# Kernel tuning notes

Hardware: AMD Instinct MI355X
Metric: run time of the kernel (lower is better)

## Reference

```python
import jax, jax.numpy as jnp
import numpy as np

N = 100000   # nodes
E = 1600000  # edges
B = 256      # graphs
EPS = 1e-5   # batchnorm eps


def setup_inputs() -> dict:
    key = jax.random.key(0)
    ks = jax.random.split(key, 20)
    inp = {
        "x": jax.random.normal(ks[0], (N, 22), dtype=jnp.float32),
        "edge_index": jax.random.randint(ks[1], (2, E), 0, N, dtype=jnp.int64),
        "batch": jnp.sort(jax.random.randint(ks[2], (N,), 0, B, dtype=jnp.int64)),
        # GCNConv weights (x @ W + b convention)
        "W1": jax.random.normal(ks[3], (22, 64), dtype=jnp.float32) * 0.2,
        "b1": jnp.zeros((64,), dtype=jnp.float32),
        "W2": jax.random.normal(ks[4], (64, 64), dtype=jnp.float32) * 0.12,
        "b2": jnp.zeros((64,), dtype=jnp.float32),
        "W3": jax.random.normal(ks[5], (64, 128), dtype=jnp.float32) * 0.12,
        "b3": jnp.zeros((128,), dtype=jnp.float32),
        # BatchNorm1d params + running stats (eval mode)
        "g1": jax.random.uniform(ks[6], (64,), minval=0.5, maxval=1.5),
        "be1": jax.random.normal(ks[7], (64,)) * 0.1,
        "m1": jax.random.normal(ks[8], (64,)) * 0.1,
        "v1": jax.random.uniform(ks[9], (64,), minval=0.5, maxval=1.5),
        "g2": jax.random.uniform(ks[10], (64,), minval=0.5, maxval=1.5),
        "be2": jax.random.normal(ks[11], (64,)) * 0.1,
        "m2": jax.random.normal(ks[12], (64,)) * 0.1,
        "v2": jax.random.uniform(ks[13], (64,), minval=0.5, maxval=1.5),
    }
    return inp


def _gcn_conv(h, W, b, src, dst, norm_e, dinv):
    # PyG GCNConv: h' = D^{-1/2}(A+I)D^{-1/2} (h W) + b
    h = h @ W                                             # [N, F]
    msg = h[src] * norm_e[:, None]                        # gather + scale [E, F]
    agg = jax.ops.segment_sum(msg, dst, num_segments=N)   # scatter-add
    agg = agg + h * dinv[:, None]                         # self-loop term
    return agg + b


def _bn_eval(x, g, be, m, v):
    return (x - m) * jax.lax.rsqrt(v + EPS) * g + be


def reference(x, edge_index, batch, W1, b1, W2, b2, W3, b3,
              g1, be1, m1, v1, g2, be2, m2, v2):
    src, dst = edge_index[0], edge_index[1]
    # degree with self-loops (computed on target nodes, symmetric norm)
    deg = jax.ops.segment_sum(jnp.ones((E,), x.dtype), dst, num_segments=N) + 1.0
    dis = jax.lax.rsqrt(deg)            # deg^{-1/2}, deg >= 1
    norm_e = dis[src] * dis[dst]        # per-edge norm
    dinv = dis * dis                    # 1/deg for self-loop edges

    h = jax.nn.relu(_bn_eval(_gcn_conv(x, W1, b1, src, dst, norm_e, dinv), g1, be1, m1, v1))
    h = jax.nn.relu(_bn_eval(_gcn_conv(h, W2, b2, src, dst, norm_e, dinv), g2, be2, m2, v2))
    h = jax.nn.relu(_gcn_conv(h, W3, b3, src, dst, norm_e, dinv))

    # global mean pool over graph ids
    sums = jax.ops.segment_sum(h, batch, num_segments=B)              # [B, 128]
    cnts = jax.ops.segment_sum(jnp.ones((N,), h.dtype), batch, num_segments=B)
    return sums / jnp.maximum(cnts, 1.0)[:, None]
```

## Files before the change

kernel.cpp:

```cpp
#include <hip/hip_runtime.h>

#define BN_EPS 1e-5f
#define EPB 4096
#define CAP 10240

typedef _Float16 half_t;
typedef _Float16 half4 __attribute__((ext_vector_type(4)));
typedef _Float16 half8 __attribute__((ext_vector_type(8)));
typedef unsigned int u32;
typedef unsigned short u16;

__device__ __forceinline__ float norm_of(u32 w) {
    u16 hb = (u16)(w & 0x7fffu);
    return (float)__builtin_bit_cast(half_t, hb);
}


__global__ void k_front(const float* __restrict__ X, half_t* __restrict__ Xh,
                        const float* __restrict__ W1, const float* __restrict__ b1,
                        const float* __restrict__ g1, const float* __restrict__ be1,
                        const float* __restrict__ m1, const float* __restrict__ v1,
                        const float* __restrict__ W2, const float* __restrict__ b2,
                        const float* __restrict__ g2, const float* __restrict__ be2,
                        const float* __restrict__ m2, const float* __restrict__ v2,
                        const float* __restrict__ W3, const float* __restrict__ b3,
                        float* __restrict__ Wp1, float* __restrict__ C1,
                        float* __restrict__ Wp2, float* __restrict__ C2,
                        float* __restrict__ Wp3, float* __restrict__ C3,
                        int* __restrict__ gcnt, float* __restrict__ sums,
                        int n, int nB) {
    int i = blockIdx.x * 256 + threadIdx.x;
    if (i < 24 * 64) {
        int r = i / 64, c = i % 64;
        float A = g1[c] * rsqrtf(v1[c] + BN_EPS);
        Wp1[i] = (r < 22) ? W1[r * 64 + c] * A : 0.0f;
        if (i < 64) C1[i] = be1[i] + (b1[i] - m1[i]) * A;
    } else if (i < 24 * 64 + 64 * 64) {
        int j = i - 24 * 64;
        int c = j % 64;
        float A = g2[c] * rsqrtf(v2[c] + BN_EPS);
        Wp2[j] = W2[j] * A;
        if (j < 64) C2[j] = be2[j] + (b2[j] - m2[j]) * A;
    } else if (i < 24 * 64 + 64 * 64 + 64 * 128) {
        int k = i - 24 * 64 - 64 * 64;
        Wp3[k] = W3[k];
        if (k < 128) C3[k] = b3[k];
    }
    if (i < 256) gcnt[i] = 0;
    if (i < nB * 128) sums[i] = 0.0f;
    if ((long long)i < (long long)n * 24) {
        int node = i / 24, c = i % 24;
        Xh[i] = (c < 22) ? (half_t)X[(size_t)node * 22 + c] : (half_t)0.0f;
    }
}


__global__ __launch_bounds__(256) void k_scatter(const int* __restrict__ src,
                                                 const int* __restrict__ dst,
                                                 int* __restrict__ gcnt,
                                                 u32* __restrict__ rec, int e) {
    __shared__ int h[256];
    __shared__ int cur[256];
    int t = threadIdx.x;
    h[t] = 0;
    __syncthreads();
    int base = blockIdx.x * EPB;
    int end = min(base + EPB, e);
    for (int i = base + t; i < end; i += 256)
        atomicAdd(&h[dst[i] >> 9], 1);
    __syncthreads();
    int c = h[t];
    cur[t] = (c > 0) ? atomicAdd(&gcnt[t], c) : 0;
    __syncthreads();
    for (int i = base + t; i < end; i += 256) {
        int d = dst[i], sv = src[i];
        int bk = d >> 9;
        int pos = atomicAdd(&cur[bk], 1);
        if (pos < CAP)
            rec[(size_t)bk * CAP + pos] = ((u32)sv << 9) | (u32)(d & 511);
    }
}


__global__ __launch_bounds__(256) void k_bmake(const u32* __restrict__ rec,
                                               const int* __restrict__ gcnt,
                                               int2* __restrict__ rp,
                                               float* __restrict__ dis,
                                               float* __restrict__ dinv, int n) {
    __shared__ int h[512];
    __shared__ int ps[256];
    int t = threadIdx.x;
    int b = blockIdx.x;
    int cnt = min(gcnt[b], CAP);
    size_t beg = (size_t)b * CAP;
    h[t] = 0; h[t + 256] = 0;
    __syncthreads();
    for (int i = t; i < cnt; i += 256)
        atomicAdd(&h[rec[beg + i] & 511], 1);
    __syncthreads();
    int d0 = h[2 * t], d1 = h[2 * t + 1];
    int pair = d0 + d1;
    ps[t] = pair;
    __syncthreads();
    int val = pair;
    for (int off = 1; off < 256; off <<= 1) {
        int tmp = (t >= off) ? ps[t - off] : 0;
        __syncthreads();
        val += tmp;
        ps[t] = val;
        __syncthreads();
    }
    int excl = (int)beg + val - pair;
    int node0 = b << 9;
    int nodeA = node0 + 2 * t, nodeB = nodeA + 1;
    if (nodeA < n) {
        rp[nodeA] = make_int2(excl, excl + d0);
        float dd = (float)(d0 + 1);
        dis[nodeA] = rsqrtf(dd);
        dinv[nodeA] = 1.0f / dd;
    }
    if (nodeB < n) {
        rp[nodeB] = make_int2(excl + d0, excl + d0 + d1);
        float dd = (float)(d1 + 1);
        dis[nodeB] = rsqrtf(dd);
        dinv[nodeB] = 1.0f / dd;
    }
}


__global__ __launch_bounds__(256) void k_bfill(const u32* __restrict__ rec,
                                               const int* __restrict__ gcnt,
                                               const int2* __restrict__ rp,
                                               const float* __restrict__ dis,
                                               u32* __restrict__ csr, int n) {
    __shared__ int cur[512];
    __shared__ float disl[512];
    int t = threadIdx.x;
    int b = blockIdx.x;
    int cnt = min(gcnt[b], CAP);
    size_t beg = (size_t)b * CAP;
    int node0 = b << 9;
    for (int j = t; j < 512; j += 256) {
        int node = node0 + j;
        cur[j] = (node < n) ? rp[node].x : 0;
        disl[j] = (node < n) ? dis[node] : 0.0f;
    }
    __syncthreads();
    for (int i = t; i < cnt; i += 256) {
        u32 r = rec[beg + i];
        int dl = r & 511;
        int s = (int)(r >> 9);
        int pos = atomicAdd(&cur[dl], 1);
        half_t hh = (half_t)(dis[s] * disl[dl]);
        csr[pos] = ((u32)s << 15) | (u32)__builtin_bit_cast(u16, hh);
    }
}


__global__ void k_gather22h(const half_t* __restrict__ Xh, const int2* __restrict__ rp,
                            const u32* __restrict__ csr, const float* __restrict__ dinv,
                            half_t* __restrict__ out, int n) {
    int node = blockIdx.x * 4 + (threadIdx.x >> 6);
    if (node >= n) return;
    int lane = threadIdx.x & 63;
    int esub = lane >> 3;
    int sub  = lane & 7;
    bool act = sub < 6;
    const half4* X4 = (const half4*)Xh;
    int2 be = rp[node];
    int beg = be.x, end = be.y;
    float di = dinv[node];
    half4 hs{};
    if (esub == 0 && act) hs = X4[(size_t)node * 6 + sub];
    float4 a0 = make_float4(0, 0, 0, 0), a1 = a0;
    for (int e = beg; e < end; e += 32) {
        int i0 = e + esub, i1 = i0 + 8, i2 = i0 + 16, i3 = i0 + 24;
        u32 w0 = csr[min(i0, end - 1)];
        u32 w1 = csr[min(i1, end - 1)];
        u32 w2 = csr[min(i2, end - 1)];
        u32 w3 = csr[min(i3, end - 1)];
        if (act && i0 < end) {
            float nn = norm_of(w0);
            half4 h = X4[(size_t)(w0 >> 15) * 6 + sub];
            a0.x = fmaf((float)h.x, nn, a0.x); a0.y = fmaf((float)h.y, nn, a0.y);
            a0.z = fmaf((float)h.z, nn, a0.z); a0.w = fmaf((float)h.w, nn, a0.w);
        }
        if (act && i1 < end) {
            float nn = norm_of(w1);
            half4 h = X4[(size_t)(w1 >> 15) * 6 + sub];
            a1.x = fmaf((float)h.x, nn, a1.x); a1.y = fmaf((float)h.y, nn, a1.y);
            a1.z = fmaf((float)h.z, nn, a1.z); a1.w = fmaf((float)h.w, nn, a1.w);
        }
        if (act && i2 < end) {
            float nn = norm_of(w2);
            half4 h = X4[(size_t)(w2 >> 15) * 6 + sub];
            a0.x = fmaf((float)h.x, nn, a0.x); a0.y = fmaf((float)h.y, nn, a0.y);
            a0.z = fmaf((float)h.z, nn, a0.z); a0.w = fmaf((float)h.w, nn, a0.w);
        }
        if (act && i3 < end) {
            float nn = norm_of(w3);
            half4 h = X4[(size_t)(w3 >> 15) * 6 + sub];
            a1.x = fmaf((float)h.x, nn, a1.x); a1.y = fmaf((float)h.y, nn, a1.y);
            a1.z = fmaf((float)h.z, nn, a1.z); a1.w = fmaf((float)h.w, nn, a1.w);
        }
    }
    float4 a;
    a.x = a0.x + a1.x; a.y = a0.y + a1.y; a.z = a0.z + a1.z; a.w = a0.w + a1.w;
#pragma unroll
    for (int d = 8; d <= 32; d <<= 1) {
        a.x += __shfl_xor(a.x, d); a.y += __shfl_xor(a.y, d);
        a.z += __shfl_xor(a.z, d); a.w += __shfl_xor(a.w, d);
    }
    if (esub == 0 && act) {
        half4 r;
        r.x = (half_t)fmaf((float)hs.x, di, a.x);
        r.y = (half_t)fmaf((float)hs.y, di, a.y);
        r.z = (half_t)fmaf((float)hs.z, di, a.z);
        r.w = (half_t)fmaf((float)hs.w, di, a.w);
        ((half4*)out)[(size_t)node * 6 + sub] = r;
    }
}

__global__ void k_gather64h(const half_t* __restrict__ H, const int2* __restrict__ rp,
                            const u32* __restrict__ csr, const float* __restrict__ dinv,
                            half_t* __restrict__ out, int n) {
    int lane = threadIdx.x & 63;
    int nsub = lane >> 5;
    int hl   = lane & 31;
    int esub = hl >> 3;
    int sub  = hl & 7;
    int node = blockIdx.x * 8 + (int)(threadIdx.x >> 6) * 2 + nsub;
    if (node >= n) return;
    const half8* H8 = (const half8*)H;
    int2 be = rp[node];
    int beg = be.x, end = be.y;
    float di = dinv[node];
    half8 hs{};
    if (esub == 0) hs = H8[(size_t)node * 8 + sub];
    float a0[8], a1[8];
#pragma unroll
    for (int j = 0; j < 8; ++j) { a0[j] = 0.0f; a1[j] = 0.0f; }
    for (int e = beg; e < end; e += 16) {
        int i0 = e + esub, i1 = i0 + 4, i2 = i0 + 8, i3 = i0 + 12;
        u32 w0 = csr[min(i0, end - 1)];
        u32 w1 = csr[min(i1, end - 1)];
        u32 w2 = csr[min(i2, end - 1)];
        u32 w3 = csr[min(i3, end - 1)];
        if (i0 < end) {
            float nn = norm_of(w0);
            half8 h = H8[(size_t)(w0 >> 15) * 8 + sub];
#pragma unroll
            for (int j = 0; j < 8; ++j) a0[j] = fmaf((float)h[j], nn, a0[j]);
        }
        if (i1 < end) {
            float nn = norm_of(w1);
            half8 h = H8[(size_t)(w1 >> 15) * 8 + sub];
#pragma unroll
            for (int j = 0; j < 8; ++j) a1[j] = fmaf((float)h[j], nn, a1[j]);
        }
        if (i2 < end) {
            float nn = norm_of(w2);
            half8 h = H8[(size_t)(w2 >> 15) * 8 + sub];
#pragma unroll
            for (int j = 0; j < 8; ++j) a0[j] = fmaf((float)h[j], nn, a0[j]);
        }
        if (i3 < end) {
            float nn = norm_of(w3);
            half8 h = H8[(size_t)(w3 >> 15) * 8 + sub];
#pragma unroll
            for (int j = 0; j < 8; ++j) a1[j] = fmaf((float)h[j], nn, a1[j]);
        }
    }
    float acc[8];
#pragma unroll
    for (int j = 0; j < 8; ++j) acc[j] = a0[j] + a1[j];
#pragma unroll
    for (int d = 8; d <= 16; d <<= 1) {
#pragma unroll
        for (int j = 0; j < 8; ++j) acc[j] += __shfl_xor(acc[j], d);
    }
    if (esub == 0) {
        half8 r;
#pragma unroll
        for (int j = 0; j < 8; ++j) r[j] = (half_t)fmaf((float)hs[j], di, acc[j]);
        ((half8*)out)[(size_t)node * 8 + sub] = r;
    }
}


template <int FIN, int FOUT>
__global__ __launch_bounds__(256) void k_gemm2(const half_t* __restrict__ P,
                                               const float* __restrict__ Wp,
                                               const float* __restrict__ Cf,
                                               half_t* __restrict__ outp, int n) {
    constexpr int COLS = FOUT / 4;
    int lane = threadIdx.x & 63;
    int part = __builtin_amdgcn_readfirstlane(threadIdx.x >> 6);
    int node = blockIdx.x * 64 + lane;
    if (node >= n) return;

    half8 xr[FIN / 8];
    const half8* p8 = (const half8*)(P + (size_t)node * FIN);
#pragma unroll
    for (int i = 0; i < FIN / 8; ++i) xr[i] = p8[i];
    const half_t* x = (const half_t*)xr;

    const float* wq = Wp + part * COLS;
    const float* cq = Cf + part * COLS;

#pragma unroll 1
    for (int c0 = 0; c0 < COLS; c0 += 16) {
        float4 a0 = make_float4(0, 0, 0, 0), a1 = a0, a2 = a0, a3 = a0;
        const float* wbase = wq + c0;
#pragma unroll
        for (int k = 0; k < FIN; ++k) {
            float xv = (float)x[k];
            const float4* wr = (const float4*)(wbase + k * FOUT);
            float4 w0 = wr[0], w1 = wr[1], w2 = wr[2], w3 = wr[3];
            a0.x = fmaf(xv, w0.x, a0.x); a0.y = fmaf(xv, w0.y, a0.y);
            a0.z = fmaf(xv, w0.z, a0.z); a0.w = fmaf(xv, w0.w, a0.w);
            a1.x = fmaf(xv, w1.x, a1.x); a1.y = fmaf(xv, w1.y, a1.y);
            a1.z = fmaf(xv, w1.z, a1.z); a1.w = fmaf(xv, w1.w, a1.w);
            a2.x = fmaf(xv, w2.x, a2.x); a2.y = fmaf(xv, w2.y, a2.y);
            a2.z = fmaf(xv, w2.z, a2.z); a2.w = fmaf(xv, w2.w, a2.w);
            a3.x = fmaf(xv, w3.x, a3.x); a3.y = fmaf(xv, w3.y, a3.y);
            a3.z = fmaf(xv, w3.z, a3.z); a3.w = fmaf(xv, w3.w, a3.w);
        }
        const float4* c4 = (const float4*)(cq + c0);
        float4 cA = c4[0], cB = c4[1], cC = c4[2], cD = c4[3];
        half8 h0, h1;
        h0[0] = (half_t)fmaxf(a0.x + cA.x, 0.0f); h0[1] = (half_t)fmaxf(a0.y + cA.y, 0.0f);
        h0[2] = (half_t)fmaxf(a0.z + cA.z, 0.0f); h0[3] = (half_t)fmaxf(a0.w + cA.w, 0.0f);
        h0[4] = (half_t)fmaxf(a1.x + cB.x, 0.0f); h0[5] = (half_t)fmaxf(a1.y + cB.y, 0.0f);
        h0[6] = (half_t)fmaxf(a1.z + cB.z, 0.0f); h0[7] = (half_t)fmaxf(a1.w + cB.w, 0.0f);
        h1[0] = (half_t)fmaxf(a2.x + cC.x, 0.0f); h1[1] = (half_t)fmaxf(a2.y + cC.y, 0.0f);
        h1[2] = (half_t)fmaxf(a2.z + cC.z, 0.0f); h1[3] = (half_t)fmaxf(a2.w + cC.w, 0.0f);
        h1[4] = (half_t)fmaxf(a3.x + cD.x, 0.0f); h1[5] = (half_t)fmaxf(a3.y + cD.y, 0.0f);
        h1[6] = (half_t)fmaxf(a3.z + cD.z, 0.0f); h1[7] = (half_t)fmaxf(a3.w + cD.w, 0.0f);
        half8* oh = (half8*)(outp + (size_t)node * FOUT + part * COLS + c0);
        oh[0] = h0;
        oh[1] = h1;
    }
}


__global__ __launch_bounds__(256) void k_gemm3pool(const half_t* __restrict__ P,
                                                   const float* __restrict__ Wp,
                                                   const float* __restrict__ Cf,
                                                   const int* __restrict__ batch,
                                                   float* __restrict__ sums, int n) {
    constexpr int FIN = 64, FOUT = 128, COLS = 32;
    __shared__ half_t tile[128][66];
    __shared__ int batl[64];
    int lane = threadIdx.x & 63;
    int part = __builtin_amdgcn_readfirstlane(threadIdx.x >> 6);
    int node = blockIdx.x * 64 + lane;
    bool valid = node < n;

    if (threadIdx.x < 64) {
        int nd = blockIdx.x * 64 + threadIdx.x;
        batl[threadIdx.x] = (nd < n) ? batch[nd] : -1;
    }

    half8 xr[FIN / 8];
    if (valid) {
        const half8* p8 = (const half8*)(P + (size_t)node * FIN);
#pragma unroll
        for (int i = 0; i < FIN / 8; ++i) xr[i] = p8[i];
    } else {
#pragma unroll
        for (int i = 0; i < FIN / 8; ++i) xr[i] = half8{};
    }
    const half_t* x = (const half_t*)xr;
    const float* wq = Wp + part * COLS;
    const float* cq = Cf + part * COLS;

#pragma unroll 1
    for (int c0 = 0; c0 < COLS; c0 += 16) {
        float4 a0 = make_float4(0, 0, 0, 0), a1 = a0, a2 = a0, a3 = a0;
        const float* wbase = wq + c0;
#pragma unroll
        for (int k = 0; k < FIN; ++k) {
            float xv = (float)x[k];
            const float4* wr = (const float4*)(wbase + k * FOUT);
            float4 w0 = wr[0], w1 = wr[1], w2 = wr[2], w3 = wr[3];
            a0.x = fmaf(xv, w0.x, a0.x); a0.y = fmaf(xv, w0.y, a0.y);
            a0.z = fmaf(xv, w0.z, a0.z); a0.w = fmaf(xv, w0.w, a0.w);
            a1.x = fmaf(xv, w1.x, a1.x); a1.y = fmaf(xv, w1.y, a1.y);
            a1.z = fmaf(xv, w1.z, a1.z); a1.w = fmaf(xv, w1.w, a1.w);
            a2.x = fmaf(xv, w2.x, a2.x); a2.y = fmaf(xv, w2.y, a2.y);
            a2.z = fmaf(xv, w2.z, a2.z); a2.w = fmaf(xv, w2.w, a2.w);
            a3.x = fmaf(xv, w3.x, a3.x); a3.y = fmaf(xv, w3.y, a3.y);
            a3.z = fmaf(xv, w3.z, a3.z); a3.w = fmaf(xv, w3.w, a3.w);
        }
        const float4* c4 = (const float4*)(cq + c0);
        float4 cA = c4[0], cB = c4[1], cC = c4[2], cD = c4[3];
        int r0 = part * COLS + c0;
        tile[r0 +  0][lane] = (half_t)fmaxf(a0.x + cA.x, 0.0f);
        tile[r0 +  1][lane] = (half_t)fmaxf(a0.y + cA.y, 0.0f);
        tile[r0 +  2][lane] = (half_t)fmaxf(a0.z + cA.z, 0.0f);
        tile[r0 +  3][lane] = (half_t)fmaxf(a0.w + cA.w, 0.0f);
        tile[r0 +  4][lane] = (half_t)fmaxf(a1.x + cB.x, 0.0f);
        tile[r0 +  5][lane] = (half_t)fmaxf(a1.y + cB.y, 0.0f);
        tile[r0 +  6][lane] = (half_t)fmaxf(a1.z + cB.z, 0.0f);
        tile[r0 +  7][lane] = (half_t)fmaxf(a1.w + cB.w, 0.0f);
        tile[r0 +  8][lane] = (half_t)fmaxf(a2.x + cC.x, 0.0f);
        tile[r0 +  9][lane] = (half_t)fmaxf(a2.y + cC.y, 0.0f);
        tile[r0 + 10][lane] = (half_t)fmaxf(a2.z + cC.z, 0.0f);
        tile[r0 + 11][lane] = (half_t)fmaxf(a2.w + cC.w, 0.0f);
        tile[r0 + 12][lane] = (half_t)fmaxf(a3.x + cD.x, 0.0f);
        tile[r0 + 13][lane] = (half_t)fmaxf(a3.y + cD.y, 0.0f);
        tile[r0 + 14][lane] = (half_t)fmaxf(a3.z + cD.z, 0.0f);
        tile[r0 + 15][lane] = (half_t)fmaxf(a3.w + cD.w, 0.0f);
    }
    __syncthreads();
    if (threadIdx.x < 128) {
        int col = threadIdx.x;
        int cur = batl[0];
        float acc = 0.0f;
        for (int i = 0; i < 64; ++i) {
            int b = batl[i];
            if (b < 0) break;
            if (b != cur) { atomicAdd(&sums[cur * 128 + col], acc); acc = 0.0f; cur = b; }
            acc += (float)tile[col][i];
        }
        if (cur >= 0) atomicAdd(&sums[cur * 128 + col], acc);
    }
}


__global__ void k_pool_div(const float* __restrict__ sums, const int* __restrict__ batch,
                           float* __restrict__ out, int n, int nB) {
    int i = blockIdx.x * blockDim.x + threadIdx.x;
    if (i >= nB * 128) return;
    int b = i >> 7;
    int lo = 0, hi = n;
    while (lo < hi) { int mid = (lo + hi) >> 1; if (batch[mid] < b) lo = mid + 1; else hi = mid; }
    int start = lo;
    lo = 0; hi = n;
    while (lo < hi) { int mid = (lo + hi) >> 1; if (batch[mid] < b + 1) lo = mid + 1; else hi = mid; }
    float cnt = (float)(lo - start);
    out[i] = sums[i] / fmaxf(cnt, 1.0f);
}


extern "C" void kernel_launch(void* const* d_in, const int* in_sizes, int n_in,
                              void* d_out, int out_size, void* d_ws, size_t ws_size,
                              hipStream_t stream) {
    const float* x   = (const float*)d_in[0];
    const int*   ei  = (const int*)d_in[1];
    const int*   bat = (const int*)d_in[2];
    const float* W1  = (const float*)d_in[3];
    const float* b1  = (const float*)d_in[4];
    const float* W2  = (const float*)d_in[5];
    const float* b2  = (const float*)d_in[6];
    const float* W3  = (const float*)d_in[7];
    const float* b3  = (const float*)d_in[8];
    const float* g1  = (const float*)d_in[9];
    const float* be1 = (const float*)d_in[10];
    const float* m1  = (const float*)d_in[11];
    const float* v1  = (const float*)d_in[12];
    const float* g2  = (const float*)d_in[13];
    const float* be2 = (const float*)d_in[14];
    const float* m2  = (const float*)d_in[15];
    const float* v2  = (const float*)d_in[16];

    const int N = in_sizes[0] / 22;
    const int E = in_sizes[1] / 2;
    const int B = out_size / 128;
    const int* src = ei;
    const int* dst = ei + E;

    const int nblk = (E + EPB - 1) / EPB;
    const int NBKT = (N + 511) >> 9;

    size_t off = 0;
    char* base = (char*)d_ws;
    auto alloc = [&](size_t bytes) -> void* {
        void* p = base + off;
        off = (off + bytes + 255) & ~(size_t)255;
        return p;
    };
    int2*   rp     = (int2*)alloc((size_t)N * 8);
    int*    gcnt   = (int*)alloc(256 * 4);
    u32*    rec    = (u32*)alloc((size_t)NBKT * CAP * 4);
    float*  dis    = (float*)alloc((size_t)N * 4);
    float*  dinv   = (float*)alloc((size_t)N * 4);
    u32*    csr    = (u32*)alloc((size_t)NBKT * CAP * 4);
    half_t* Xh     = (half_t*)alloc((size_t)N * 24 * 2);
    half_t* Hh1    = (half_t*)alloc((size_t)N * 64 * 2);
    half_t* Hh2    = (half_t*)alloc((size_t)N * 64 * 2);
    half_t* aggH   = (half_t*)alloc((size_t)N * 64 * 2);
    float*  sums   = (float*)alloc((size_t)B * 128 * 4);
    float*  Wp1    = (float*)alloc(24 * 64 * 4);
    float*  Wp2    = (float*)alloc(64 * 64 * 4);
    float*  Wp3    = (float*)alloc(64 * 128 * 4);
    float*  C1     = (float*)alloc(64 * 4);
    float*  C2     = (float*)alloc(64 * 4);
    float*  C3     = (float*)alloc(128 * 4);

    const int T = 256;
    auto blk = [](long long n, int t) { return (int)((n + t - 1) / t); };

    int gf = blk((long long)N * 24, T);
    int gf2 = blk(24 * 64 + 64 * 64 + 64 * 128, T);
    int gf3 = blk((long long)B * 128, T);
    if (gf2 > gf) gf = gf2;
    if (gf3 > gf) gf = gf3;

    k_front<<<gf, T, 0, stream>>>(x, Xh, W1, b1, g1, be1, m1, v1,
                                  W2, b2, g2, be2, m2, v2, W3, b3,
                                  Wp1, C1, Wp2, C2, Wp3, C3, gcnt, sums, N, B);

    k_scatter<<<nblk, T, 0, stream>>>(src, dst, gcnt, rec, E);
    k_bmake<<<NBKT, T, 0, stream>>>(rec, gcnt, rp, dis, dinv, N);
    k_bfill<<<NBKT, T, 0, stream>>>(rec, gcnt, rp, dis, csr, N);

    k_gather22h<<<blk(N, 4), T, 0, stream>>>(Xh, rp, csr, dinv, aggH, N);
    k_gemm2<24, 64><<<blk(N, 64), T, 0, stream>>>(aggH, Wp1, C1, Hh1, N);

    k_gather64h<<<blk(N, 8), T, 0, stream>>>(Hh1, rp, csr, dinv, aggH, N);
    k_gemm2<64, 64><<<blk(N, 64), T, 0, stream>>>(aggH, Wp2, C2, Hh2, N);

    k_gather64h<<<blk(N, 8), T, 0, stream>>>(Hh2, rp, csr, dinv, aggH, N);
    k_gemm3pool<<<blk(N, 64), T, 0, stream>>>(aggH, Wp3, C3, bat, sums, N);

    k_pool_div<<<blk((long long)B * 128, T), T, 0, stream>>>(sums, bat, (float*)d_out, N, B);
}
```

Measured before the change: 323.4 us.

## Replace scalar FMA node GEMMs with MFMA using split-fp16 weights

The three per-node dense transforms move from scalar fp32 FMA loops to MFMA 16x16x32 f16 instructions. Weights are pre-split into high and low fp16 parts and pre-swizzled into the MFMA B-operand layout in the front kernel, which keeps near-fp32 weight precision at the cost of two MFMAs per step. This targets the ALU-bound GEMM kernels. The output writes become per-element scattered half stores instead of vectorized half8 stores.

```diff
diff --git a/kernel.cpp b/kernel.cpp
--- a/kernel.cpp
+++ b/kernel.cpp
@@ -7,6 +7,7 @@
 typedef _Float16 half_t;
 typedef _Float16 half4 __attribute__((ext_vector_type(4)));
 typedef _Float16 half8 __attribute__((ext_vector_type(8)));
+typedef float f32x4 __attribute__((ext_vector_type(4)));
 typedef unsigned int u32;
 typedef unsigned short u16;
 
@@ -24,30 +25,56 @@
                         const float* __restrict__ g2, const float* __restrict__ be2,
                         const float* __restrict__ m2, const float* __restrict__ v2,
                         const float* __restrict__ W3, const float* __restrict__ b3,
-                        float* __restrict__ Wp1, float* __restrict__ C1,
-                        float* __restrict__ Wp2, float* __restrict__ C2,
-                        float* __restrict__ Wp3, float* __restrict__ C3,
+                        half_t* __restrict__ B1h, half_t* __restrict__ B1l,
+                        half_t* __restrict__ B2h, half_t* __restrict__ B2l,
+                        half_t* __restrict__ B3h, half_t* __restrict__ B3l,
+                        float* __restrict__ C1, float* __restrict__ C2,
+                        float* __restrict__ C3,
                         int* __restrict__ gcnt, float* __restrict__ sums,
                         int n, int nB) {
     int i = blockIdx.x * 256 + threadIdx.x;
-    if (i < 24 * 64) {
-        int r = i / 64, c = i % 64;
-        float A = g1[c] * rsqrtf(v1[c] + BN_EPS);
-        Wp1[i] = (r < 22) ? W1[r * 64 + c] * A : 0.0f;
-        if (i < 64) C1[i] = be1[i] + (b1[i] - m1[i]) * A;
-    } else if (i < 24 * 64 + 64 * 64) {
-        int j = i - 24 * 64;
-        int c = j % 64;
+    if (i < 64) {
+        float A = g1[i] * rsqrtf(v1[i] + BN_EPS);
+        C1[i] = be1[i] + (b1[i] - m1[i]) * A;
+    } else if (i < 128) {
+        int c = i - 64;
         float A = g2[c] * rsqrtf(v2[c] + BN_EPS);
-        Wp2[j] = W2[j] * A;
-        if (j < 64) C2[j] = be2[j] + (b2[j] - m2[j]) * A;
-    } else if (i < 24 * 64 + 64 * 64 + 64 * 128) {
-        int k = i - 24 * 64 - 64 * 64;
-        Wp3[k] = W3[k];
-        if (k < 128) C3[k] = b3[k];
+        C2[c] = be2[c] + (b2[c] - m2[c]) * A;
+    } else if (i < 256) {
+        int c = i - 128;
+        C3[c] = b3[c];
     }
     if (i < 256) gcnt[i] = 0;
     if (i < nB * 128) sums[i] = 0.0f;
+    int e = i - 256;
+    if (e >= 0 && e < 2048) {
+        int j = e & 7, l = (e >> 3) & 63, t = e >> 9;
+        int k = ((l >> 4) << 3) + j;
+        int col = t * 16 + (l & 15);
+        float A = g1[col] * rsqrtf(v1[col] + BN_EPS);
+        float w = (k < 22) ? W1[k * 64 + col] * A : 0.0f;
+        half_t wh = (half_t)w;
+        B1h[e] = wh; B1l[e] = (half_t)(w - (float)wh);
+    } else if (e >= 2048 && e < 6144) {
+        int e2 = e - 2048;
+        int j = e2 & 7, l = (e2 >> 3) & 63, rest = e2 >> 9;
+        int s = rest & 1, t = rest >> 1;
+        int k = s * 32 + ((l >> 4) << 3) + j;
+        int col = t * 16 + (l & 15);
+        float A = g2[col] * rsqrtf(v2[col] + BN_EPS);
+        float w = W2[k * 64 + col] * A;
+        half_t wh = (half_t)w;
+        B2h[e2] = wh; B2l[e2] = (half_t)(w - (float)wh);
+    } else if (e >= 6144 && e < 14336) {
+        int e3 = e - 6144;
+        int j = e3 & 7, l = (e3 >> 3) & 63, rest = e3 >> 9;
+        int s = rest & 1, t = rest >> 1;
+        int k = s * 32 + ((l >> 4) << 3) + j;
+        int col = t * 16 + (l & 15);
+        float w = W3[k * 128 + col];
+        half_t wh = (half_t)w;
+        B3h[e3] = wh; B3l[e3] = (half_t)(w - (float)wh);
+    }
     if ((long long)i < (long long)n * 24) {
         int node = i / 24, c = i % 24;
         Xh[i] = (c < 22) ? (half_t)X[(size_t)node * 22 + c] : (half_t)0.0f;
@@ -288,130 +315,93 @@
 }
 
 
-template <int FIN, int FOUT>
-__global__ __launch_bounds__(256) void k_gemm2(const half_t* __restrict__ P,
-                                               const float* __restrict__ Wp,
+template <int FIN, int KS, int FOUT>
+__global__ __launch_bounds__(256) void k_mgemm(const half_t* __restrict__ P,
+                                               const half_t* __restrict__ Bh,
+                                               const half_t* __restrict__ Bl,
                                                const float* __restrict__ Cf,
                                                half_t* __restrict__ outp, int n) {
-    constexpr int COLS = FOUT / 4;
     int lane = threadIdx.x & 63;
-    int part = __builtin_amdgcn_readfirstlane(threadIdx.x >> 6);
-    int node = blockIdx.x * 64 + lane;
-    if (node >= n) return;
-
-    half8 xr[FIN / 8];
-    const half8* p8 = (const half8*)(P + (size_t)node * FIN);
-#pragma unroll
-    for (int i = 0; i < FIN / 8; ++i) xr[i] = p8[i];
-    const half_t* x = (const half_t*)xr;
-
-    const float* wq = Wp + part * COLS;
-    const float* cq = Cf + part * COLS;
-
-#pragma unroll 1
-    for (int c0 = 0; c0 < COLS; c0 += 16) {
-        float4 a0 = make_float4(0, 0, 0, 0), a1 = a0, a2 = a0, a3 = a0;
-        const float* wbase = wq + c0;
-#pragma unroll
-        for (int k = 0; k < FIN; ++k) {
-            float xv = (float)x[k];
-            const float4* wr = (const float4*)(wbase + k * FOUT);
-            float4 w0 = wr[0], w1 = wr[1], w2 = wr[2], w3 = wr[3];
-            a0.x = fmaf(xv, w0.x, a0.x); a0.y = fmaf(xv, w0.y, a0.y);
-            a0.z = fmaf(xv, w0.z, a0.z); a0.w = fmaf(xv, w0.w, a0.w);
-            a1.x = fmaf(xv, w1.x, a1.x); a1.y = fmaf(xv, w1.y, a1.y);
-            a1.z = fmaf(xv, w1.z, a1.z); a1.w = fmaf(xv, w1.w, a1.w);
-            a2.x = fmaf(xv, w2.x, a2.x); a2.y = fmaf(xv, w2.y, a2.y);
-            a2.z = fmaf(xv, w2.z, a2.z); a2.w = fmaf(xv, w2.w, a2.w);
-            a3.x = fmaf(xv, w3.x, a3.x); a3.y = fmaf(xv, w3.y, a3.y);
-            a3.z = fmaf(xv, w3.z, a3.z); a3.w = fmaf(xv, w3.w, a3.w);
-        }
-        const float4* c4 = (const float4*)(cq + c0);
-        float4 cA = c4[0], cB = c4[1], cC = c4[2], cD = c4[3];
-        half8 h0, h1;
-        h0[0] = (half_t)fmaxf(a0.x + cA.x, 0.0f); h0[1] = (half_t)fmaxf(a0.y + cA.y, 0.0f);
-        h0[2] = (half_t)fmaxf(a0.z + cA.z, 0.0f); h0[3] = (half_t)fmaxf(a0.w + cA.w, 0.0f);
-        h0[4] = (half_t)fmaxf(a1.x + cB.x, 0.0f); h0[5] = (half_t)fmaxf(a1.y + cB.y, 0.0f);
-        h0[6] = (half_t)fmaxf(a1.z + cB.z, 0.0f); h0[7] = (half_t)fmaxf(a1.w + cB.w, 0.0f);
-        h1[0] = (half_t)fmaxf(a2.x + cC.x, 0.0f); h1[1] = (half_t)fmaxf(a2.y + cC.y, 0.0f);
-        h1[2] = (half_t)fmaxf(a2.z + cC.z, 0.0f); h1[3] = (half_t)fmaxf(a2.w + cC.w, 0.0f);
-        h1[4] = (half_t)fmaxf(a3.x + cD.x, 0.0f); h1[5] = (half_t)fmaxf(a3.y + cD.y, 0.0f);
-        h1[6] = (half_t)fmaxf(a3.z + cD.z, 0.0f); h1[7] = (half_t)fmaxf(a3.w + cD.w, 0.0f);
-        half8* oh = (half8*)(outp + (size_t)node * FOUT + part * COLS + c0);
-        oh[0] = h0;
-        oh[1] = h1;
-    }
-}
-
-
-__global__ __launch_bounds__(256) void k_gemm3pool(const half_t* __restrict__ P,
-                                                   const float* __restrict__ Wp,
-                                                   const float* __restrict__ Cf,
-                                                   const int* __restrict__ batch,
-                                                   float* __restrict__ sums, int n) {
-    constexpr int FIN = 64, FOUT = 128, COLS = 32;
+    int wv = threadIdx.x >> 6;
+    int node0 = blockIdx.x * 64 + wv * 16;
+    int arow = lane & 15, kg = lane >> 4;
+    int node = node0 + arow;
+    bool v = node < n;
+
+    half8 a[KS];
+#pragma unroll
+    for (int s = 0; s < KS; ++s) {
+        bool ld = v && (FIN == 64 || kg < 3);
+        a[s] = ld ? *(const half8*)(P + (size_t)node * FIN + s * 32 + kg * 8) : half8{};
+    }
+
+    constexpr int NT = FOUT / 16;
+    const half8* BH = (const half8*)Bh;
+    const half8* BL = (const half8*)Bl;
+    int colb = lane & 15;
+#pragma unroll
+    for (int t = 0; t < NT; ++t) {
+        float cinit = Cf[t * 16 + colb];
+        f32x4 acc = {cinit, cinit, cinit, cinit};
+#pragma unroll
+        for (int s = 0; s < KS; ++s) {
+            half8 bh = BH[(t * KS + s) * 64 + lane];
+            half8 bl = BL[(t * KS + s) * 64 + lane];
+            acc = __builtin_amdgcn_mfma_f32_16x16x32_f16(a[s], bh, acc, 0, 0, 0);
+            acc = __builtin_amdgcn_mfma_f32_16x16x32_f16(a[s], bl, acc, 0, 0, 0);
+        }
+#pragma unroll
+        for (int r = 0; r < 4; ++r) {
+            int nd = node0 + kg * 4 + r;
+            if (nd < n)
+                outp[(size_t)nd * FOUT + t * 16 + colb] = (half_t)fmaxf(acc[r], 0.0f);
+        }
+    }
+}
+
+
+__global__ __launch_bounds__(256) void k_mgemm3pool(const half_t* __restrict__ P,
+                                                    const half_t* __restrict__ Bh,
+                                                    const half_t* __restrict__ Bl,
+                                                    const float* __restrict__ Cf,
+                                                    const int* __restrict__ batch,
+                                                    float* __restrict__ sums, int n) {
     __shared__ half_t tile[128][66];
     __shared__ int batl[64];
     int lane = threadIdx.x & 63;
-    int part = __builtin_amdgcn_readfirstlane(threadIdx.x >> 6);
-    int node = blockIdx.x * 64 + lane;
-    bool valid = node < n;
+    int wv = threadIdx.x >> 6;
+    int node0 = blockIdx.x * 64 + wv * 16;
+    int arow = lane & 15, kg = lane >> 4;
+    int node = node0 + arow;
+    bool v = node < n;
 
     if (threadIdx.x < 64) {
         int nd = blockIdx.x * 64 + threadIdx.x;
         batl[threadIdx.x] = (nd < n) ? batch[nd] : -1;
     }
 
-    half8 xr[FIN / 8];
-    if (valid) {
-        const half8* p8 = (const half8*)(P + (size_t)node * FIN);
-#pragma unroll
-        for (int i = 0; i < FIN / 8; ++i) xr[i] = p8[i];
-    } else {
-#pragma unroll
-        for (int i = 0; i < FIN / 8; ++i) xr[i] = half8{};
-    }
-    const half_t* x = (const half_t*)xr;
-    const float* wq = Wp + part * COLS;
-    const float* cq = Cf + part * COLS;
-
-#pragma unroll 1
-    for (int c0 = 0; c0 < COLS; c0 += 16) {
-        float4 a0 = make_float4(0, 0, 0, 0), a1 = a0, a2 = a0, a3 = a0;
-        const float* wbase = wq + c0;
-#pragma unroll
-        for (int k = 0; k < FIN; ++k) {
-            float xv = (float)x[k];
-            const float4* wr = (const float4*)(wbase + k * FOUT);
-            float4 w0 = wr[0], w1 = wr[1], w2 = wr[2], w3 = wr[3];
-            a0.x = fmaf(xv, w0.x, a0.x); a0.y = fmaf(xv, w0.y, a0.y);
-            a0.z = fmaf(xv, w0.z, a0.z); a0.w = fmaf(xv, w0.w, a0.w);
-            a1.x = fmaf(xv, w1.x, a1.x); a1.y = fmaf(xv, w1.y, a1.y);
-            a1.z = fmaf(xv, w1.z, a1.z); a1.w = fmaf(xv, w1.w, a1.w);
-            a2.x = fmaf(xv, w2.x, a2.x); a2.y = fmaf(xv, w2.y, a2.y);
-            a2.z = fmaf(xv, w2.z, a2.z); a2.w = fmaf(xv, w2.w, a2.w);
-            a3.x = fmaf(xv, w3.x, a3.x); a3.y = fmaf(xv, w3.y, a3.y);
-            a3.z = fmaf(xv, w3.z, a3.z); a3.w = fmaf(xv, w3.w, a3.w);
-        }
-        const float4* c4 = (const float4*)(cq + c0);
-        float4 cA = c4[0], cB = c4[1], cC = c4[2], cD = c4[3];
-        int r0 = part * COLS + c0;
-        tile[r0 +  0][lane] = (half_t)fmaxf(a0.x + cA.x, 0.0f);
-        tile[r0 +  1][lane] = (half_t)fmaxf(a0.y + cA.y, 0.0f);
-        tile[r0 +  2][lane] = (half_t)fmaxf(a0.z + cA.z, 0.0f);
-        tile[r0 +  3][lane] = (half_t)fmaxf(a0.w + cA.w, 0.0f);
-        tile[r0 +  4][lane] = (half_t)fmaxf(a1.x + cB.x, 0.0f);
-        tile[r0 +  5][lane] = (half_t)fmaxf(a1.y + cB.y, 0.0f);
-        tile[r0 +  6][lane] = (half_t)fmaxf(a1.z + cB.z, 0.0f);
-        tile[r0 +  7][lane] = (half_t)fmaxf(a1.w + cB.w, 0.0f);
-        tile[r0 +  8][lane] = (half_t)fmaxf(a2.x + cC.x, 0.0f);
-        tile[r0 +  9][lane] = (half_t)fmaxf(a2.y + cC.y, 0.0f);
-        tile[r0 + 10][lane] = (half_t)fmaxf(a2.z + cC.z, 0.0f);
-        tile[r0 + 11][lane] = (half_t)fmaxf(a2.w + cC.w, 0.0f);
-        tile[r0 + 12][lane] = (half_t)fmaxf(a3.x + cD.x, 0.0f);
-        tile[r0 + 13][lane] = (half_t)fmaxf(a3.y + cD.y, 0.0f);
-        tile[r0 + 14][lane] = (half_t)fmaxf(a3.z + cD.z, 0.0f);
-        tile[r0 + 15][lane] = (half_t)fmaxf(a3.w + cD.w, 0.0f);
+    half8 a[2];
+#pragma unroll
+    for (int s = 0; s < 2; ++s)
+        a[s] = v ? *(const half8*)(P + (size_t)node * 64 + s * 32 + kg * 8) : half8{};
+
+    const half8* BH = (const half8*)Bh;
+    const half8* BL = (const half8*)Bl;
+    int colb = lane & 15;
+#pragma unroll
+    for (int t = 0; t < 8; ++t) {
+        float cinit = Cf[t * 16 + colb];
+        f32x4 acc = {cinit, cinit, cinit, cinit};
+#pragma unroll
+        for (int s = 0; s < 2; ++s) {
+            half8 bh = BH[(t * 2 + s) * 64 + lane];
+            half8 bl = BL[(t * 2 + s) * 64 + lane];
+            acc = __builtin_amdgcn_mfma_f32_16x16x32_f16(a[s], bh, acc, 0, 0, 0);
+            acc = __builtin_amdgcn_mfma_f32_16x16x32_f16(a[s], bl, acc, 0, 0, 0);
+        }
+#pragma unroll
+        for (int r = 0; r < 4; ++r)
+            tile[t * 16 + colb][wv * 16 + kg * 4 + r] = (half_t)fmaxf(acc[r], 0.0f);
     }
     __syncthreads();
     if (threadIdx.x < 128) {
@@ -492,9 +482,12 @@
     half_t* Hh2    = (half_t*)alloc((size_t)N * 64 * 2);
     half_t* aggH   = (half_t*)alloc((size_t)N * 64 * 2);
     float*  sums   = (float*)alloc((size_t)B * 128 * 4);
-    float*  Wp1    = (float*)alloc(24 * 64 * 4);
-    float*  Wp2    = (float*)alloc(64 * 64 * 4);
-    float*  Wp3    = (float*)alloc(64 * 128 * 4);
+    half_t* B1h    = (half_t*)alloc(2048 * 2);
+    half_t* B1l    = (half_t*)alloc(2048 * 2);
+    half_t* B2h    = (half_t*)alloc(4096 * 2);
+    half_t* B2l    = (half_t*)alloc(4096 * 2);
+    half_t* B3h    = (half_t*)alloc(8192 * 2);
+    half_t* B3l    = (half_t*)alloc(8192 * 2);
     float*  C1     = (float*)alloc(64 * 4);
     float*  C2     = (float*)alloc(64 * 4);
     float*  C3     = (float*)alloc(128 * 4);
@@ -503,27 +496,28 @@
     auto blk = [](long long n, int t) { return (int)((n + t - 1) / t); };
 
     int gf = blk((long long)N * 24, T);
-    int gf2 = blk(24 * 64 + 64 * 64 + 64 * 128, T);
+    int gf2 = blk(256 + 14336, T);
     int gf3 = blk((long long)B * 128, T);
     if (gf2 > gf) gf = gf2;
     if (gf3 > gf) gf = gf3;
 
     k_front<<<gf, T, 0, stream>>>(x, Xh, W1, b1, g1, be1, m1, v1,
                                   W2, b2, g2, be2, m2, v2, W3, b3,
-                                  Wp1, C1, Wp2, C2, Wp3, C3, gcnt, sums, N, B);
+                                  B1h, B1l, B2h, B2l, B3h, B3l,
+                                  C1, C2, C3, gcnt, sums, N, B);
 
     k_scatter<<<nblk, T, 0, stream>>>(src, dst, gcnt, rec, E);
     k_bmake<<<NBKT, T, 0, stream>>>(rec, gcnt, rp, dis, dinv, N);
     k_bfill<<<NBKT, T, 0, stream>>>(rec, gcnt, rp, dis, csr, N);
 
     k_gather22h<<<blk(N, 4), T, 0, stream>>>(Xh, rp, csr, dinv, aggH, N);
-    k_gemm2<24, 64><<<blk(N, 64), T, 0, stream>>>(aggH, Wp1, C1, Hh1, N);
+    k_mgemm<24, 1, 64><<<blk(N, 64), T, 0, stream>>>(aggH, B1h, B1l, C1, Hh1, N);
 
     k_gather64h<<<blk(N, 8), T, 0, stream>>>(Hh1, rp, csr, dinv, aggH, N);
-    k_gemm2<64, 64><<<blk(N, 64), T, 0, stream>>>(aggH, Wp2, C2, Hh2, N);
+    k_mgemm<64, 2, 64><<<blk(N, 64), T, 0, stream>>>(aggH, B2h, B2l, C2, Hh2, N);
 
     k_gather64h<<<blk(N, 8), T, 0, stream>>>(Hh2, rp, csr, dinv, aggH, N);
-    k_gemm3pool<<<blk(N, 64), T, 0, stream>>>(aggH, Wp3, C3, bat, sums, N);
+    k_mgemm3pool<<<blk(N, 64), T, 0, stream>>>(aggH, B3h, B3l, C3, bat, sums, N);
 
     k_pool_div<<<blk((long long)B * 128, T), T, 0, stream>>>(sums, bat, (float*)d_out, N, B);
 }
```

Measured after the change: 292.3 us. -9.6%, faster.
